# Kernel optimization log

Measured on AMD Instinct MI355X. Metric: run time of the kernel, lower is better.

## Reference

```python
import jax, jax.numpy as jnp
import numpy as np

H = 16   # num_attention_heads
G = 4    # num_gqa_groups
D = 64   # head_dim = hidden // H
HIDDEN = 1024
KV_DIM = HIDDEN // H * G  # 256
EPS = 1e-5


def setup_inputs() -> dict:
    key = jax.random.key(0)
    k0, k1, k2, k3 = jax.random.split(key, 4)
    x = jax.random.normal(k0, (8, 4096, HIDDEN), dtype=jnp.float32)
    query_weight = jax.random.normal(k1, (HIDDEN, HIDDEN), dtype=jnp.float32) * 0.02
    key_weight = jax.random.normal(k2, (KV_DIM, HIDDEN), dtype=jnp.float32) * 0.02
    value_weight = jax.random.normal(k3, (KV_DIM, HIDDEN), dtype=jnp.float32) * 0.02
    return {
        "x": x,
        "query_weight": query_weight,
        "key_weight": key_weight,
        "value_weight": value_weight,
        "query_bias": jnp.zeros((HIDDEN,), jnp.float32),
        "key_bias": jnp.zeros((KV_DIM,), jnp.float32),
        "value_bias": jnp.zeros((KV_DIM,), jnp.float32),
        "layer_norm_weight": jnp.ones((HIDDEN,), jnp.float32),
        "layer_norm_bias": jnp.zeros((HIDDEN,), jnp.float32),
    }


def reference(x, query_weight, key_weight, value_weight, query_bias, key_bias,
              value_bias, layer_norm_weight, layer_norm_bias):
    b, s, _ = x.shape
    # Shared LayerNorm (q is k is v path in apply_qkv_norm)
    mu = jnp.mean(x, axis=-1, keepdims=True)
    var = jnp.mean(jnp.square(x - mu), axis=-1, keepdims=True)
    xn = (x - mu) * jax.lax.rsqrt(var + EPS) * layer_norm_weight + layer_norm_bias
    # Q/K/V projections (F.linear: x @ W.T + b)
    q = xn @ query_weight.T + query_bias           # [b, s, H*D]
    k = xn @ key_weight.T + key_bias               # [b, s, G*1*D]
    v = xn @ value_weight.T + value_bias           # [b, s, G*1*D]
    # 'b s (h d) -> b h s d'
    q = q.reshape(b, s, H, D).transpose(0, 2, 1, 3)           # [b, H, s, D]
    # 'b s (g h d) -> b h (g s) d' with h = KV_DIM//(G*D) = 1
    def kv_rearrange(t):
        t = t.reshape(b, s, G, 1, D)                          # b s g h d
        t = t.transpose(0, 3, 2, 1, 4)                        # b h g s d
        return t.reshape(b, 1, G * s, D)                      # [b, 1, G*s, D]
    return q, kv_rearrange(k), kv_rearrange(v)
```

## Files before the change

kernel.cpp:

```cpp
#include <hip/hip_runtime.h>
#include <hip/hip_bf16.h>


#define HIDDEN 1024
#define NTOK   32768

typedef __bf16 bf16x8 __attribute__((ext_vector_type(8)));
typedef float  f32x4  __attribute__((ext_vector_type(4)));

#define GLOBAL_AS(p) ((const __attribute__((address_space(1))) void*)(p))
#define LDS_AS(p)    ((__attribute__((address_space(3))) void*)(p))

__device__ __forceinline__ unsigned short f2bf(float f) {
  union { float f; unsigned int i; } x; x.f = f;
  unsigned int r = x.i + 0x7FFFu + ((x.i >> 16) & 1u);
  return (unsigned short)(r >> 16);
}

__global__ __launch_bounds__(256) void ln_kernel(
    const float* __restrict__ x,
    const float* __restrict__ gamma,
    const float* __restrict__ beta,
    unsigned short* __restrict__ xn) {
  const int row = blockIdx.x;
  const int t   = threadIdx.x;
  const size_t base = (size_t)row * HIDDEN;

  const float4 v = ((const float4*)(x + base))[t];
  float s  = v.x + v.y + v.z + v.w;
  float s2 = v.x*v.x + v.y*v.y + v.z*v.z + v.w*v.w;
#pragma unroll
  for (int off = 32; off >= 1; off >>= 1) {
    s  += __shfl_xor(s,  off);
    s2 += __shfl_xor(s2, off);
  }
  __shared__ float red[8];
  const int w = t >> 6;
  if ((t & 63) == 0) { red[w] = s; red[4 + w] = s2; }
  __syncthreads();
  s  = red[0] + red[1] + red[2] + red[3];
  s2 = red[4] + red[5] + red[6] + red[7];
  const float mu   = s * (1.0f / HIDDEN);
  const float rstd = rsqrtf(s2 * (1.0f / HIDDEN) - mu * mu + 1e-5f);

  const float4 g  = ((const float4*)gamma)[t];
  const float4 bb = ((const float4*)beta)[t];
  ushort4 o;
  o.x = f2bf((v.x - mu) * rstd * g.x + bb.x);
  o.y = f2bf((v.y - mu) * rstd * g.y + bb.y);
  o.z = f2bf((v.z - mu) * rstd * g.z + bb.z);
  o.w = f2bf((v.w - mu) * rstd * g.w + bb.w);
  ((ushort4*)(xn + base))[t] = o;
}

__global__ __launch_bounds__(256) void cvt_kernel(
    const float* __restrict__ src, unsigned short* __restrict__ dst) {
  const int i = blockIdx.x * 256 + threadIdx.x;
  const float4 v = ((const float4*)src)[i];
  ushort4 o;
  o.x = f2bf(v.x); o.y = f2bf(v.y); o.z = f2bf(v.z); o.w = f2bf(v.w);
  ((ushort4*)dst)[i] = o;
}

__global__ __launch_bounds__(512, 2) void qkv_gemm(
    const unsigned short* __restrict__ xn,
    const unsigned short* __restrict__ wq,
    const unsigned short* __restrict__ wk,
    const unsigned short* __restrict__ wv,
    const float* __restrict__ bq,
    const float* __restrict__ bk,
    const float* __restrict__ bv,
    float* __restrict__ out) {
  __shared__ unsigned short Alds[32768];
  __shared__ unsigned short Blds[32768];

  const int bid = blockIdx.x;
  const int swz = (bid & 7) * 96 + (bid >> 3);
  const int mt  = swz / 6;
  const int nt  = swz % 6;
  const int brow = mt * 256;

  const unsigned short* wbase; const float* biasptr;
  int segcol; size_t obase; int hg;
  if (nt < 4)       { wbase = wq + (size_t)nt * 256 * HIDDEN; biasptr = bq; segcol = nt * 256; obase = 0u;        hg = 16; }
  else if (nt == 4) { wbase = wk;                             biasptr = bk; segcol = 0;        obase = 33554432u; hg = 4;  }
  else              { wbase = wv;                             biasptr = bv; segcol = 0;        obase = 41943040u; hg = 4;  }

  const int t = threadIdx.x;
  const int w = t >> 6, lane = t & 63;
  const int wm = w >> 2, wn = w & 3;
  const int l15 = lane & 15, hi = lane >> 4;

  const int sr  = 2 * w * 16 + (lane >> 2);
  const int scg = ((lane & 3) ^ ((lane >> 3) & 3)) * 8;
  const unsigned short* aST = xn    + (size_t)(brow + sr) * HIDDEN + scg;
  const unsigned short* bST = wbase + (size_t)sr * HIDDEN + scg;
  const int ldsq = 2 * w * 512;

  const int rdx  = (hi ^ ((l15 >> 1) & 3)) * 8;
  const int rowA = wm * 128 + l15;
  const int rowB = wn * 64  + l15;

  f32x4 acc[8][4];
#pragma unroll
  for (int m = 0; m < 8; ++m)
#pragma unroll
    for (int n = 0; n < 4; ++n) acc[m][n] = (f32x4){0.f, 0.f, 0.f, 0.f};
  bf16x8 a[8], b[2];

#define STA(BUF, KK, KT) do {                                                   \
    unsigned short* _d = Alds + (BUF) * 16384 + (KK) * 8192 + ldsq;             \
    const unsigned short* _s = aST + (size_t)((KT) * 64 + (KK) * 32);           \
    __builtin_amdgcn_global_load_lds(GLOBAL_AS(_s), LDS_AS(_d), 16, 0, 0);      \
    __builtin_amdgcn_global_load_lds(GLOBAL_AS(_s + 16 * HIDDEN), LDS_AS(_d + 512), 16, 0, 0); \
  } while (0)
#define STB(BUF, KK, KT) do {                                                   \
    unsigned short* _d = Blds + (BUF) * 16384 + (KK) * 8192 + ldsq;             \
    const unsigned short* _s = bST + (size_t)((KT) * 64 + (KK) * 32);           \
    __builtin_amdgcn_global_load_lds(GLOBAL_AS(_s), LDS_AS(_d), 16, 0, 0);      \
    __builtin_amdgcn_global_load_lds(GLOBAL_AS(_s + 16 * HIDDEN), LDS_AS(_d + 512), 16, 0, 0); \
  } while (0)
#define DSA(BUF, KK) do { _Pragma("unroll")                                     \
    for (int m = 0; m < 8; ++m)                                                 \
      a[m] = *(const bf16x8*)(Alds + (BUF) * 16384 + (KK) * 8192 + (rowA + m * 16) * 32 + rdx); \
  } while (0)
#define DSB(BUF, KK, NB) do { _Pragma("unroll")                                 \
    for (int n = 0; n < 2; ++n)                                                 \
      b[n] = *(const bf16x8*)(Blds + (BUF) * 16384 + (KK) * 8192 + (rowB + ((NB) + n) * 16) * 32 + rdx); \
  } while (0)
#define MM(NB) do {                                                             \
    __builtin_amdgcn_s_setprio(1);                                              \
    _Pragma("unroll") for (int m = 0; m < 8; ++m) {                             \
      acc[m][(NB)]     = __builtin_amdgcn_mfma_f32_16x16x32_bf16(a[m], b[0], acc[m][(NB)], 0, 0, 0);     \
      acc[m][(NB) + 1] = __builtin_amdgcn_mfma_f32_16x16x32_bf16(a[m], b[1], acc[m][(NB) + 1], 0, 0, 0); \
    }                                                                           \
    __builtin_amdgcn_s_setprio(0);                                              \
  } while (0)
#define BARS do { __builtin_amdgcn_s_barrier();                                 \
    asm volatile("s_waitcnt lgkmcnt(0)" ::: "memory");                          \
    __builtin_amdgcn_sched_barrier(0); } while (0)
#define ENDB do { __builtin_amdgcn_s_barrier();                                 \
    __builtin_amdgcn_sched_barrier(0); } while (0)
#define VMW(N) asm volatile("s_waitcnt vmcnt(" #N ")" ::: "memory")

  STA(0, 0, 0); STB(0, 0, 0); STA(0, 1, 0); STB(0, 1, 0);
  STA(1, 0, 1); STB(1, 0, 1); STA(1, 1, 1);
  VMW(10);
  __builtin_amdgcn_s_barrier();
  __builtin_amdgcn_sched_barrier(0);

  for (int i = 0; i < 7; ++i) {
    const int T = 2 * i;
     DSA(0, 0); DSB(0, 0, 0); STB(1, 1, T + 1); BARS; MM(0);          ENDB;
     DSB(0, 0, 2);            STA(0, 0, T + 2); BARS; MM(2); VMW(10); ENDB;
     DSA(0, 1); DSB(0, 1, 0); STB(0, 0, T + 2); BARS; MM(0);          ENDB;
     DSB(0, 1, 2);            STA(0, 1, T + 2); BARS; MM(2); VMW(10); ENDB;
     DSA(1, 0); DSB(1, 0, 0); STB(0, 1, T + 2); BARS; MM(0);          ENDB;
     DSB(1, 0, 2);            STA(1, 0, T + 3); BARS; MM(2); VMW(10); ENDB;
     DSA(1, 1); DSB(1, 1, 0); STB(1, 0, T + 3); BARS; MM(0);          ENDB;
     DSB(1, 1, 2);            STA(1, 1, T + 3); BARS; MM(2); VMW(10); ENDB;
  }
   DSA(0, 0); DSB(0, 0, 0); STB(1, 1, 15); BARS; MM(0);         ENDB;
   DSB(0, 0, 2);                           BARS; MM(2); VMW(8); ENDB;
   DSA(0, 1); DSB(0, 1, 0);                BARS; MM(0);         ENDB;
   DSB(0, 1, 2);                           BARS; MM(2); VMW(4); ENDB;
   DSA(1, 0); DSB(1, 0, 0);                BARS; MM(0);         ENDB;
   DSB(1, 0, 2);                           BARS; MM(2); VMW(0); ENDB;
   DSA(1, 1); DSB(1, 1, 0);                BARS; MM(0);         ENDB;
   DSB(1, 1, 2);                           BARS; MM(2);         ENDB;

#undef STA
#undef STB
#undef DSA
#undef DSB
#undef MM
#undef BARS
#undef ENDB
#undef VMW

  float* ep = (float*)Alds;
  const int epb = w * 1344;
  const int headcol = segcol + wn * 64;
  const int gidx = headcol >> 6;
  const int tok0 = brow + wm * 128;
  const int b_ = tok0 >> 12;
  float* wout = out + obase + (size_t)(b_ * hg + gidx) * 262144u
                    + (size_t)(tok0 & 4095) * 64u;
  float biasv[4];
#pragma unroll
  for (int n = 0; n < 4; ++n) biasv[n] = biasptr[headcol + n * 16 + l15];

#pragma unroll
  for (int m = 0; m < 8; ++m) {
#pragma unroll
    for (int n = 0; n < 4; ++n)
#pragma unroll
      for (int j = 0; j < 4; ++j)
        ep[epb + (hi * 4 + j) * 84 + n * 16 + l15] = acc[m][n][j] + biasv[n];
    asm volatile("s_waitcnt lgkmcnt(0)" ::: "memory");
#pragma unroll
    for (int it = 0; it < 4; ++it) {
      const int r = it * 4 + hi;
      const float4 v = *(const float4*)(ep + epb + r * 84 + l15 * 4);
      *(float4*)(wout + (size_t)(m * 16 + r) * 64 + l15 * 4) = v;
    }
  }
}

extern "C" void kernel_launch(void* const* d_in, const int* in_sizes, int n_in,
                              void* d_out, int out_size, void* d_ws, size_t ws_size,
                              hipStream_t stream) {
  const float* x  = (const float*)d_in[0];
  const float* wq = (const float*)d_in[1];
  const float* wk = (const float*)d_in[2];
  const float* wv = (const float*)d_in[3];
  const float* bq = (const float*)d_in[4];
  const float* bk = (const float*)d_in[5];
  const float* bv = (const float*)d_in[6];
  const float* g  = (const float*)d_in[7];
  const float* be = (const float*)d_in[8];
  float* out = (float*)d_out;

  unsigned short* xn  = (unsigned short*)d_ws;
  unsigned short* wqb = (unsigned short*)((char*)d_ws + (64u << 20));
  unsigned short* wkb = wqb + 1024 * 1024;
  unsigned short* wvb = wkb + 256 * 1024;

  ln_kernel<<<NTOK, 256, 0, stream>>>(x, g, be, xn);
  cvt_kernel<<<1024, 256, 0, stream>>>(wq, wqb);
  cvt_kernel<<<256,  256, 0, stream>>>(wk, wkb);
  cvt_kernel<<<256,  256, 0, stream>>>(wv, wvb);
  qkv_gemm<<<768, 512, 0, stream>>>(xn, wqb, wkb, wvb, bq, bk, bv, out);
}
```

Baseline: 176.5 us.

## Fuse LayerNorm with weight conversion and restructure GEMM main loop to ping-pong fragments

Measured after the change: 171.2 us. -3.0%, faster.

```diff
diff --git a/kernel.cpp b/kernel.cpp
--- a/kernel.cpp
+++ b/kernel.cpp
@@ -17,56 +17,60 @@
   return (unsigned short)(r >> 16);
 }
 
-__global__ __launch_bounds__(256) void ln_kernel(
+__global__ __launch_bounds__(256) void ln_cvt_kernel(
     const float* __restrict__ x,
     const float* __restrict__ gamma,
     const float* __restrict__ beta,
-    unsigned short* __restrict__ xn) {
-  const int row = blockIdx.x;
+    const float* __restrict__ wq,
+    const float* __restrict__ wk,
+    const float* __restrict__ wv,
+    unsigned short* __restrict__ xn,
+    unsigned short* __restrict__ wb) {
+  const int bid = blockIdx.x;
   const int t   = threadIdx.x;
-  const size_t base = (size_t)row * HIDDEN;
-
-  const float4 v = ((const float4*)(x + base))[t];
-  float s  = v.x + v.y + v.z + v.w;
-  float s2 = v.x*v.x + v.y*v.y + v.z*v.z + v.w*v.w;
-#pragma unroll
-  for (int off = 32; off >= 1; off >>= 1) {
-    s  += __shfl_xor(s,  off);
-    s2 += __shfl_xor(s2, off);
+  if (bid < NTOK) {
+    const size_t base = (size_t)bid * HIDDEN;
+    const float4 v = ((const float4*)(x + base))[t];
+    float s  = v.x + v.y + v.z + v.w;
+    float s2 = v.x*v.x + v.y*v.y + v.z*v.z + v.w*v.w;
+#pragma unroll
+    for (int off = 32; off >= 1; off >>= 1) {
+      s  += __shfl_xor(s,  off);
+      s2 += __shfl_xor(s2, off);
+    }
+    __shared__ float red[8];
+    const int w = t >> 6;
+    if ((t & 63) == 0) { red[w] = s; red[4 + w] = s2; }
+    __syncthreads();
+    s  = red[0] + red[1] + red[2] + red[3];
+    s2 = red[4] + red[5] + red[6] + red[7];
+    const float mu   = s * (1.0f / HIDDEN);
+    const float rstd = rsqrtf(s2 * (1.0f / HIDDEN) - mu * mu + 1e-5f);
+    const float4 g  = ((const float4*)gamma)[t];
+    const float4 bb = ((const float4*)beta)[t];
+    ushort4 o;
+    o.x = f2bf((v.x - mu) * rstd * g.x + bb.x);
+    o.y = f2bf((v.y - mu) * rstd * g.y + bb.y);
+    o.z = f2bf((v.z - mu) * rstd * g.z + bb.z);
+    o.w = f2bf((v.w - mu) * rstd * g.w + bb.w);
+    ((ushort4*)(xn + base))[t] = o;
+  } else {
+    const int b2 = bid - NTOK;
+    const float* src;
+    int off;
+    if (b2 < 1024)      { src = wq; off = b2; }
+    else if (b2 < 1280) { src = wk; off = b2 - 1024; }
+    else                { src = wv; off = b2 - 1280; }
+    const float4 v = ((const float4*)src)[off * 256 + t];
+    ushort4 o;
+    o.x = f2bf(v.x); o.y = f2bf(v.y); o.z = f2bf(v.z); o.w = f2bf(v.w);
+    ((ushort4*)wb)[b2 * 256 + t] = o;
   }
-  __shared__ float red[8];
-  const int w = t >> 6;
-  if ((t & 63) == 0) { red[w] = s; red[4 + w] = s2; }
-  __syncthreads();
-  s  = red[0] + red[1] + red[2] + red[3];
-  s2 = red[4] + red[5] + red[6] + red[7];
-  const float mu   = s * (1.0f / HIDDEN);
-  const float rstd = rsqrtf(s2 * (1.0f / HIDDEN) - mu * mu + 1e-5f);
-
-  const float4 g  = ((const float4*)gamma)[t];
-  const float4 bb = ((const float4*)beta)[t];
-  ushort4 o;
-  o.x = f2bf((v.x - mu) * rstd * g.x + bb.x);
-  o.y = f2bf((v.y - mu) * rstd * g.y + bb.y);
-  o.z = f2bf((v.z - mu) * rstd * g.z + bb.z);
-  o.w = f2bf((v.w - mu) * rstd * g.w + bb.w);
-  ((ushort4*)(xn + base))[t] = o;
-}
-
-__global__ __launch_bounds__(256) void cvt_kernel(
-    const float* __restrict__ src, unsigned short* __restrict__ dst) {
-  const int i = blockIdx.x * 256 + threadIdx.x;
-  const float4 v = ((const float4*)src)[i];
-  ushort4 o;
-  o.x = f2bf(v.x); o.y = f2bf(v.y); o.z = f2bf(v.z); o.w = f2bf(v.w);
-  ((ushort4*)dst)[i] = o;
 }
 
 __global__ __launch_bounds__(512, 2) void qkv_gemm(
     const unsigned short* __restrict__ xn,
-    const unsigned short* __restrict__ wq,
-    const unsigned short* __restrict__ wk,
-    const unsigned short* __restrict__ wv,
+    const unsigned short* __restrict__ wqb,
     const float* __restrict__ bq,
     const float* __restrict__ bk,
     const float* __restrict__ bv,
@@ -82,9 +86,9 @@
 
   const unsigned short* wbase; const float* biasptr;
   int segcol; size_t obase; int hg;
-  if (nt < 4)       { wbase = wq + (size_t)nt * 256 * HIDDEN; biasptr = bq; segcol = nt * 256; obase = 0u;        hg = 16; }
-  else if (nt == 4) { wbase = wk;                             biasptr = bk; segcol = 0;        obase = 33554432u; hg = 4;  }
-  else              { wbase = wv;                             biasptr = bv; segcol = 0;        obase = 41943040u; hg = 4;  }
+  if (nt < 4)       { wbase = wqb + (size_t)nt * 256 * HIDDEN;  biasptr = bq; segcol = nt * 256; obase = 0u;        hg = 16; }
+  else if (nt == 4) { wbase = wqb + (size_t)1024 * HIDDEN;      biasptr = bk; segcol = 0;        obase = 33554432u; hg = 4;  }
+  else              { wbase = wqb + (size_t)1280 * HIDDEN;      biasptr = bv; segcol = 0;        obase = 41943040u; hg = 4;  }
 
   const int t = threadIdx.x;
   const int w = t >> 6, lane = t & 63;
@@ -106,7 +110,7 @@
   for (int m = 0; m < 8; ++m)
 #pragma unroll
     for (int n = 0; n < 4; ++n) acc[m][n] = (f32x4){0.f, 0.f, 0.f, 0.f};
-  bf16x8 a[8], b[2];
+  bf16x8 a0[4], a1[4], b0[4], b1[4];
 
 #define STA(BUF, KK, KT) do {                                                   \
     unsigned short* _d = Alds + (BUF) * 16384 + (KK) * 8192 + ldsq;             \
@@ -120,63 +124,68 @@
     __builtin_amdgcn_global_load_lds(GLOBAL_AS(_s), LDS_AS(_d), 16, 0, 0);      \
     __builtin_amdgcn_global_load_lds(GLOBAL_AS(_s + 16 * HIDDEN), LDS_AS(_d + 512), 16, 0, 0); \
   } while (0)
-#define DSA(BUF, KK) do { _Pragma("unroll")                                     \
-    for (int m = 0; m < 8; ++m)                                                 \
-      a[m] = *(const bf16x8*)(Alds + (BUF) * 16384 + (KK) * 8192 + (rowA + m * 16) * 32 + rdx); \
-  } while (0)
-#define DSB(BUF, KK, NB) do { _Pragma("unroll")                                 \
-    for (int n = 0; n < 2; ++n)                                                 \
-      b[n] = *(const bf16x8*)(Blds + (BUF) * 16384 + (KK) * 8192 + (rowB + ((NB) + n) * 16) * 32 + rdx); \
-  } while (0)
-#define MM(NB) do {                                                             \
+#define RDA(SET, BUF, KK, MH) do { _Pragma("unroll")                            \
+    for (int m = 0; m < 4; ++m)                                                 \
+      SET[m] = *(const bf16x8*)(Alds + (BUF) * 16384 + (KK) * 8192 + (rowA + (MH) * 64 + m * 16) * 32 + rdx); \
+  } while (0)
+#define RDB(SET, BUF, KK) do { _Pragma("unroll")                                \
+    for (int n = 0; n < 4; ++n)                                                 \
+      SET[n] = *(const bf16x8*)(Blds + (BUF) * 16384 + (KK) * 8192 + (rowB + n * 16) * 32 + rdx); \
+  } while (0)
+#define MMX(ASET, BSET, MH) do {                                                \
     __builtin_amdgcn_s_setprio(1);                                              \
-    _Pragma("unroll") for (int m = 0; m < 8; ++m) {                             \
-      acc[m][(NB)]     = __builtin_amdgcn_mfma_f32_16x16x32_bf16(a[m], b[0], acc[m][(NB)], 0, 0, 0);     \
-      acc[m][(NB) + 1] = __builtin_amdgcn_mfma_f32_16x16x32_bf16(a[m], b[1], acc[m][(NB) + 1], 0, 0, 0); \
-    }                                                                           \
+    _Pragma("unroll") for (int m = 0; m < 4; ++m)                               \
+      _Pragma("unroll") for (int n = 0; n < 4; ++n)                             \
+        acc[(MH) * 4 + m][n] = __builtin_amdgcn_mfma_f32_16x16x32_bf16(ASET[m], BSET[n], acc[(MH) * 4 + m][n], 0, 0, 0); \
     __builtin_amdgcn_s_setprio(0);                                              \
   } while (0)
-#define BARS do { __builtin_amdgcn_s_barrier();                                 \
+#define ENDPH(VMN) do {                                                         \
     asm volatile("s_waitcnt lgkmcnt(0)" ::: "memory");                          \
-    __builtin_amdgcn_sched_barrier(0); } while (0)
-#define ENDB do { __builtin_amdgcn_s_barrier();                                 \
-    __builtin_amdgcn_sched_barrier(0); } while (0)
-#define VMW(N) asm volatile("s_waitcnt vmcnt(" #N ")" ::: "memory")
+    asm volatile("s_waitcnt vmcnt(" #VMN ")" ::: "memory");                     \
+    __builtin_amdgcn_sched_barrier(0);                                          \
+    __builtin_amdgcn_s_barrier();                                               \
+    __builtin_amdgcn_sched_barrier(0);                                          \
+  } while (0)
 
   STA(0, 0, 0); STB(0, 0, 0); STA(0, 1, 0); STB(0, 1, 0);
-  STA(1, 0, 1); STB(1, 0, 1); STA(1, 1, 1);
-  VMW(10);
+  STA(1, 0, 1); STB(1, 0, 1); STA(1, 1, 1); STB(1, 1, 1);
+  asm volatile("s_waitcnt vmcnt(12)" ::: "memory");
+  __builtin_amdgcn_sched_barrier(0);
+  __builtin_amdgcn_s_barrier();
+  __builtin_amdgcn_sched_barrier(0);
+  RDA(a0, 0, 0, 0); RDB(b0, 0, 0);
+  asm volatile("s_waitcnt lgkmcnt(0)" ::: "memory");
+  __builtin_amdgcn_sched_barrier(0);
   __builtin_amdgcn_s_barrier();
   __builtin_amdgcn_sched_barrier(0);
 
   for (int i = 0; i < 7; ++i) {
     const int T = 2 * i;
-     DSA(0, 0); DSB(0, 0, 0); STB(1, 1, T + 1); BARS; MM(0);          ENDB;
-     DSB(0, 0, 2);            STA(0, 0, T + 2); BARS; MM(2); VMW(10); ENDB;
-     DSA(0, 1); DSB(0, 1, 0); STB(0, 0, T + 2); BARS; MM(0);          ENDB;
-     DSB(0, 1, 2);            STA(0, 1, T + 2); BARS; MM(2); VMW(10); ENDB;
-     DSA(1, 0); DSB(1, 0, 0); STB(0, 1, T + 2); BARS; MM(0);          ENDB;
-     DSB(1, 0, 2);            STA(1, 0, T + 3); BARS; MM(2); VMW(10); ENDB;
-     DSA(1, 1); DSB(1, 1, 0); STB(1, 0, T + 3); BARS; MM(0);          ENDB;
-     DSB(1, 1, 2);            STA(1, 1, T + 3); BARS; MM(2); VMW(10); ENDB;
+     STB(0, 0, T + 2); RDA(a1, 0, 0, 1);                  MMX(a0, b0, 0); ENDPH(10);
+     STA(0, 0, T + 2); RDA(a0, 0, 1, 0); RDB(b1, 0, 1);   MMX(a1, b0, 1); ENDPH(10);
+     STB(0, 1, T + 2); RDA(a1, 0, 1, 1);                  MMX(a0, b1, 0); ENDPH(10);
+     STA(0, 1, T + 2); RDA(a0, 1, 0, 0); RDB(b0, 1, 0);   MMX(a1, b1, 1); ENDPH(10);
+     STB(1, 0, T + 3); RDA(a1, 1, 0, 1);                  MMX(a0, b0, 0); ENDPH(10);
+     STA(1, 0, T + 3); RDA(a0, 1, 1, 0); RDB(b1, 1, 1);   MMX(a1, b0, 1); ENDPH(10);
+     STB(1, 1, T + 3); RDA(a1, 1, 1, 1);                  MMX(a0, b1, 0); ENDPH(10);
+     STA(1, 1, T + 3); RDA(a0, 0, 0, 0); RDB(b0, 0, 0);   MMX(a1, b1, 1); ENDPH(10);
   }
-   DSA(0, 0); DSB(0, 0, 0); STB(1, 1, 15); BARS; MM(0);         ENDB;
-   DSB(0, 0, 2);                           BARS; MM(2); VMW(8); ENDB;
-   DSA(0, 1); DSB(0, 1, 0);                BARS; MM(0);         ENDB;
-   DSB(0, 1, 2);                           BARS; MM(2); VMW(4); ENDB;
-   DSA(1, 0); DSB(1, 0, 0);                BARS; MM(0);         ENDB;
-   DSB(1, 0, 2);                           BARS; MM(2); VMW(0); ENDB;
-   DSA(1, 1); DSB(1, 1, 0);                BARS; MM(0);         ENDB;
-   DSB(1, 1, 2);                           BARS; MM(2);         ENDB;
+   RDA(a1, 0, 0, 1);                  MMX(a0, b0, 0); ENDPH(8);
+   RDA(a0, 0, 1, 0); RDB(b1, 0, 1);   MMX(a1, b0, 1); ENDPH(6);
+   RDA(a1, 0, 1, 1);                  MMX(a0, b1, 0); ENDPH(4);
+   RDA(a0, 1, 0, 0); RDB(b0, 1, 0);   MMX(a1, b1, 1); ENDPH(2);
+   RDA(a1, 1, 0, 1);                  MMX(a0, b0, 0); ENDPH(0);
+   RDA(a0, 1, 1, 0); RDB(b1, 1, 1);   MMX(a1, b0, 1); ENDPH(0);
+   RDA(a1, 1, 1, 1);                  MMX(a0, b1, 0); ENDPH(0);
+                                      MMX(a1, b1, 1);
+  asm volatile("s_waitcnt lgkmcnt(0)" ::: "memory");
 
 #undef STA
 #undef STB
-#undef DSA
-#undef DSB
-#undef MM
-#undef BARS
-#undef ENDB
-#undef VMW
+#undef RDA
+#undef RDB
+#undef MMX
+#undef ENDPH
 
   float* ep = (float*)Alds;
   const int epb = w * 1344;
@@ -221,14 +230,9 @@
   const float* be = (const float*)d_in[8];
   float* out = (float*)d_out;
 
-  unsigned short* xn  = (unsigned short*)d_ws;
-  unsigned short* wqb = (unsigned short*)((char*)d_ws + (64u << 20));
-  unsigned short* wkb = wqb + 1024 * 1024;
-  unsigned short* wvb = wkb + 256 * 1024;
-
-  ln_kernel<<<NTOK, 256, 0, stream>>>(x, g, be, xn);
-  cvt_kernel<<<1024, 256, 0, stream>>>(wq, wqb);
-  cvt_kernel<<<256,  256, 0, stream>>>(wk, wkb);
-  cvt_kernel<<<256,  256, 0, stream>>>(wv, wvb);
-  qkv_gemm<<<768, 512, 0, stream>>>(xn, wqb, wkb, wvb, bq, bk, bv, out);
-}
+  unsigned short* xn = (unsigned short*)d_ws;
+  unsigned short* wb = (unsigned short*)((char*)d_ws + (64u << 20));
+
+  ln_cvt_kernel<<<NTOK + 1536, 256, 0, stream>>>(x, g, be, wq, wk, wv, xn, wb);
+  qkv_gemm<<<768, 512, 0, stream>>>(xn, wb, bq, bk, bv, out);
+}
```
